# Performance work log

Hardware: AMD Instinct MI355X
Metric: run time of the kernel (lower is better)

## Reference

```python
import jax, jax.numpy as jnp
import numpy as np

NUM_EXPERTS = 8
AUX_LOSS_COEF = 0.01


def setup_inputs() -> dict:
    key = jax.random.key(0)
    ks = jax.random.split(key, 5)
    B, S, D, E, H = 4, 2048, 1024, NUM_EXPERTS, 4096
    scale = 0.02  # typical init scale so gelu/softmax stay in sane ranges
    return {
        "hidden_states": jax.random.normal(ks[0], (B, S, D), dtype=jnp.float32),
        "router_w": jax.random.normal(ks[1], (D, E), dtype=jnp.float32) * scale,
        "router_b": jnp.zeros((E,), dtype=jnp.float32),
        "w1": jax.random.normal(ks[2], (E, D, H), dtype=jnp.float32) * scale,
        "b1": jnp.zeros((E, H), dtype=jnp.float32),
        "w2": jax.random.normal(ks[3], (E, H, D), dtype=jnp.float32) * scale,
        "b2": jnp.zeros((E, D), dtype=jnp.float32),
    }


def reference(hidden_states, router_w, router_b, w1, b1, w2, b2):
    B, S, D = hidden_states.shape
    E = w1.shape[0]
    x = hidden_states.reshape(-1, D)  # [T, D] flattened tokens

    # Switch router: top-1 expert, combine weight = softmax prob of chosen expert
    logits = x @ router_w + router_b                      # [T, E]
    probs = jax.nn.softmax(logits, axis=-1)               # [T, E]
    sel = jnp.argmax(logits, axis=-1)                     # [T] int
    gate = jnp.take_along_axis(probs, sel[:, None], axis=1)[:, 0]  # [T]

    # Expert FFNs: per-expert Linear -> gelu -> Linear, masked top-1 combine.
    # Loop is over the small fixed expert count (structurally distinct weights).
    out = jnp.zeros_like(x)
    for e in range(E):
        h = jax.nn.gelu(x @ w1[e] + b1[e])                # [T, H]
        ye = h @ w2[e] + b2[e]                            # [T, D]
        mask = (sel == e).astype(x.dtype)
        out = out + (mask * gate)[:, None] * ye

    # Switch load-balancing auxiliary loss
    mean_probs = probs.mean(axis=0)                       # [E]
    assignments = jnp.mean(jax.nn.one_hot(sel, E, dtype=x.dtype), axis=0)  # [E]
    aux_loss = jnp.sum(mean_probs * assignments) * E
    total_loss = AUX_LOSS_COEF * aux_loss

    return out.reshape(B, S, D), total_loss
```

## Files before the change

kernel.cpp:

```cpp
#include <hip/hip_runtime.h>
#include <cstdint>

typedef __bf16 bf16_t;
typedef __attribute__((ext_vector_type(8))) __bf16 bf16x8;
typedef __attribute__((ext_vector_type(4))) float f32x4;
typedef unsigned short ushort_t;

#define TOKENS 8192
#define DIM 1024
#define HID 4096
#define NEXP 8


__device__ __forceinline__ void gl_lds16(const void* g, void* l) {
  __builtin_amdgcn_global_load_lds(
      (__attribute__((address_space(1))) void*)(void*)g,
      (__attribute__((address_space(3))) void*)l, 16, 0, 0);
}

__device__ __forceinline__ float gelu_fast(float x) {
  float x2 = x * x;
  float z2 = x * (1.59576912f + 0.07135482f * x2);
  float e = __expf(-z2);
  return x * __builtin_amdgcn_rcpf(1.f + e);
}

template <int N>
__device__ __forceinline__ void pwait() {
  __builtin_amdgcn_sched_barrier(0);
  if constexpr (N == 4) asm volatile("s_waitcnt vmcnt(4)" ::: "memory");
  else asm volatile("s_waitcnt vmcnt(0)" ::: "memory");
  __builtin_amdgcn_sched_barrier(0);
  __builtin_amdgcn_s_barrier();
  __builtin_amdgcn_sched_barrier(0);
}

__device__ __forceinline__ int xcd_chunk(int f, int nwg) {
  int q = nwg >> 3, r = nwg & 7;
  int xcd = f & 7, pos = f >> 3;
  return (xcd < r) ? (xcd * (q + 1) + pos) : (r * (q + 1) + (xcd - r) * q + pos);
}

__global__ void router_kernel(const float* __restrict__ x, const float* __restrict__ rw,
                              const float* __restrict__ rbias, bf16_t* __restrict__ xb,
                              int* __restrict__ sel, float* __restrict__ gate,
                              float* __restrict__ pprob, int* __restrict__ pcnt) {
  __shared__ float sprob[NEXP];
  __shared__ int scnt[NEXP];
  int t = threadIdx.x, lane = t & 63, wave = t >> 6;
  if (t < NEXP) { sprob[t] = 0.f; scnt[t] = 0; }
  __syncthreads();
  int tok = blockIdx.x * 4 + wave;
  const float* xp = x + (size_t)tok * DIM + lane * 16;
  float acc[NEXP];
#pragma unroll
  for (int e = 0; e < NEXP; ++e) acc[e] = 0.f;
  ushort_t xv[16];
#pragma unroll
  for (int j = 0; j < 16; j += 4) {
    float4 v = *(const float4*)(xp + j);
    const float* wr = rw + (size_t)(lane * 16 + j) * NEXP;
    float c[4] = {v.x, v.y, v.z, v.w};
#pragma unroll
    for (int d = 0; d < 4; ++d) {
      xv[j + d] = __builtin_bit_cast(ushort_t, (bf16_t)c[d]);
#pragma unroll
      for (int e = 0; e < NEXP; ++e) acc[e] += c[d] * wr[d * NEXP + e];
    }
  }
  {
    uint4* xop = (uint4*)(xb + (size_t)tok * DIM + lane * 16);
    xop[0] = ((uint4*)xv)[0];
    xop[1] = ((uint4*)xv)[1];
  }
#pragma unroll
  for (int s = 1; s < 64; s <<= 1)
#pragma unroll
    for (int e = 0; e < NEXP; ++e) acc[e] += __shfl_xor(acc[e], s);
  if (lane == 0) {
    float lg[NEXP];
#pragma unroll
    for (int e = 0; e < NEXP; ++e) lg[e] = acc[e] + rbias[e];
    float mx = lg[0]; int am = 0;
#pragma unroll
    for (int e = 1; e < NEXP; ++e) if (lg[e] > mx) { mx = lg[e]; am = e; }
    float p[NEXP]; float se = 0.f;
#pragma unroll
    for (int e = 0; e < NEXP; ++e) { p[e] = __expf(lg[e] - mx); se += p[e]; }
    float inv = 1.f / se;
#pragma unroll
    for (int e = 0; e < NEXP; ++e) { p[e] *= inv; atomicAdd(&sprob[e], p[e]); }
    sel[tok] = am;
    gate[tok] = p[am];
    atomicAdd(&scnt[am], 1);
  }
  __syncthreads();
  if (t < NEXP) {
    pprob[blockIdx.x * NEXP + t] = sprob[t];
    pcnt[blockIdx.x * NEXP + t] = scnt[t];
  }
}

__global__ void tcvt2_kernel(const float* __restrict__ w1, const float* __restrict__ w2,
                             bf16_t* __restrict__ w1t, bf16_t* __restrict__ w2t) {
  __shared__ float tile[64][65];
  int y = blockIdx.y;
  int which = y >> 3, e = y & 7;
  int R = which ? HID : DIM;
  int C = which ? DIM : HID;
  const float* src = (which ? w2 : w1) + (size_t)e * R * C;
  bf16_t* dst = (which ? w2t : w1t) + (size_t)e * R * C;
  int cbt = C >> 6;
  int rt = blockIdx.x / cbt, ct = blockIdx.x % cbt;
  int rb = rt * 64, cb = ct * 64;
  int t = threadIdx.x;
  int r = t >> 2, cq = (t & 3) * 16;
  const float* sp = src + (size_t)(rb + r) * C + cb + cq;
#pragma unroll
  for (int j = 0; j < 16; j += 4) {
    float4 v = *(const float4*)(sp + j);
    tile[r][cq + j + 0] = v.x; tile[r][cq + j + 1] = v.y;
    tile[r][cq + j + 2] = v.z; tile[r][cq + j + 3] = v.w;
  }
  __syncthreads();
  int oc = t >> 2, orr = (t & 3) * 16;
  ushort_t tmp[16];
#pragma unroll
  for (int j = 0; j < 16; ++j) {
    bf16_t b = (bf16_t)tile[orr + j][oc];
    tmp[j] = __builtin_bit_cast(ushort_t, b);
  }
  uint4* dp = (uint4*)(dst + (size_t)(cb + oc) * R + rb + orr);
  dp[0] = ((uint4*)tmp)[0];
  dp[1] = ((uint4*)tmp)[1];
}

__global__ void reduce_kernel(const float* __restrict__ pprob, const int* __restrict__ pcnt,
                              int nb, int* __restrict__ meta, float* __restrict__ loss_out) {
  __shared__ float fred[256];
  __shared__ int ired[256];
  int t = threadIdx.x;
  int e = t & 7, i0 = t >> 3;
  float fs = 0.f; int is = 0;
  for (int i = i0; i < nb; i += 32) { fs += pprob[i * 8 + e]; is += pcnt[i * 8 + e]; }
  fred[t] = fs; ired[t] = is;
  __syncthreads();
  if (t < NEXP) {
    float tp = 0.f; int tc = 0;
    for (int j = 0; j < 32; ++j) { tp += fred[j * 8 + t]; tc += ired[j * 8 + t]; }
    meta[t] = tc;
    fred[t] = tp;
    meta[16 + t] = 0;
  }
  __syncthreads();
  if (t == 0) {
    int off = 0; float loss = 0.f; int s2 = 0;
    for (int q = 0; q < NEXP; ++q) {
      int c = meta[q];
      meta[8 + q] = off;
      int nt2 = (c + 127) >> 7;
      for (int m = 0; m < nt2; ++m) meta[96 + s2++] = (q << 16) | m;
      off += c;
      loss += (fred[q] / (float)TOKENS) * ((float)c / (float)TOKENS);
    }
    meta[25] = s2;
    *loss_out = loss * (float)NEXP * 0.01f;
  }
}

__global__ void scatter_kernel(const int* __restrict__ sel, int* __restrict__ meta,
                               int* __restrict__ idxl) {
  int tok = blockIdx.x * 256 + threadIdx.x;
  int lane = threadIdx.x & 63;
  int e = sel[tok];
  const int* offsets = meta + 8;
  int* cursors = meta + 16;
#pragma unroll
  for (int ex = 0; ex < NEXP; ++ex) {
    unsigned long long mask = __ballot(e == ex);
    if (e == ex) {
      int leader = __ffsll(mask) - 1;
      int total = __popcll(mask);
      int rank = __popcll(mask & ((1ull << lane) - 1ull));
      int base = 0;
      if (lane == leader) base = atomicAdd(&cursors[ex], total);
      base = __shfl(base, leader);
      idxl[offsets[ex] + base + rank] = tok;
    }
  }
}

#define STG(Q, KT) do {                                                      \
    int _kb = (KT) * 32;                                                     \
    gl_lds16(apA0 + _kb, L + (Q) * 8192 + wave * 512);                       \
    gl_lds16(apA1 + _kb, L + (Q) * 8192 + 2048 + wave * 512);                 \
    gl_lds16(bpB0 + _kb, L + (Q) * 8192 + 4096 + wave * 512);                 \
    gl_lds16(bpB1 + _kb, L + (Q) * 8192 + 6144 + wave * 512);                 \
  } while (0)

#define CMP(Q) do {                                                          \
    const bf16_t* Ab = L + (Q) * 8192;                                       \
    const bf16_t* Bb = Ab + 4096;                                            \
    bf16x8 af[4], bv[4];                                                     \
    _Pragma("unroll")                                                        \
    for (int m = 0; m < 4; ++m)                                              \
      af[m] = *(const bf16x8*)&Ab[(wrow * 64 + m * 16 + l15) * 32 + ks];     \
    _Pragma("unroll")                                                        \
    for (int n = 0; n < 4; ++n)                                              \
      bv[n] = *(const bf16x8*)&Bb[(wcol * 64 + n * 16 + l15) * 32 + ks];     \
    __builtin_amdgcn_s_setprio(1);                                           \
    _Pragma("unroll")                                                        \
    for (int m = 0; m < 4; ++m)                                              \
      _Pragma("unroll")                                                      \
      for (int n = 0; n < 4; ++n)                                            \
        acc[m][n] = __builtin_amdgcn_mfma_f32_16x16x32_bf16(af[m], bv[n], acc[m][n], 0, 0, 0); \
    __builtin_amdgcn_s_setprio(0);                                           \
  } while (0)

__global__ __launch_bounds__(256, 3) void gemm1_kernel(
    const bf16_t* __restrict__ xb, const bf16_t* __restrict__ w1t,
    const float* __restrict__ b1, const int* __restrict__ idxl,
    const int* __restrict__ meta, bf16_t* __restrict__ h) {
  int S = gridDim.x;
  int f = blockIdx.y * S + blockIdx.x;
  int lf = xcd_chunk(f, S * gridDim.y);
  int slot = lf % S, nt = lf / S;
  if (slot >= meta[25]) return;
  int tm = meta[96 + slot];
  int e = tm >> 16, mt = tm & 0xffff;
  int cnt = meta[e];
  int off = meta[8 + e];
  int mBase = mt * 128;
  int nBase = nt * 128;
  __shared__ bf16_t L[24576];
  int t = threadIdx.x, lane = t & 63, wave = t >> 6;
  int l15 = lane & 15, g = lane >> 4;
  int wrow = wave >> 1, wcol = wave & 1;
  int ks = (g ^ (l15 & 3)) * 8;
  f32x4 acc[4][4];
#pragma unroll
  for (int m = 0; m < 4; ++m)
#pragma unroll
    for (int n = 0; n < 4; ++n) acc[m][n] = (f32x4){0.f, 0.f, 0.f, 0.f};

  int srow = t >> 2;
  int koff = ((t & 3) ^ (srow & 3)) * 8;
  int c1 = cnt - 1;
  int sA0 = mBase + srow; sA0 = sA0 < c1 ? sA0 : c1;
  int sA1 = mBase + 64 + srow; sA1 = sA1 < c1 ? sA1 : c1;
  const bf16_t* apA0 = xb + (size_t)idxl[off + sA0] * DIM + koff;
  const bf16_t* apA1 = xb + (size_t)idxl[off + sA1] * DIM + koff;
  const bf16_t* wb = w1t + (size_t)e * HID * DIM;
  const bf16_t* bpB0 = wb + (size_t)(nBase + srow) * DIM + koff;
  const bf16_t* bpB1 = wb + (size_t)(nBase + 64 + srow) * DIM + koff;

  STG(0, 0);
  STG(1, 1);
  pwait<4>();
#pragma unroll 1
  for (int kt = 0; kt < 30; kt += 3) {
    STG(2, kt + 2); CMP(0); pwait<4>();
    STG(0, kt + 3); CMP(1); pwait<4>();
    STG(1, kt + 4); CMP(2); pwait<4>();
  }
  CMP(0);
  pwait<0>();
  CMP(1);

  float bias[4];
#pragma unroll
  for (int n = 0; n < 4; ++n) bias[n] = b1[e * HID + nBase + wcol * 64 + n * 16 + l15];
#pragma unroll
  for (int m = 0; m < 4; ++m) {
    int rb0 = mBase + wrow * 64 + m * 16 + g * 4;
#pragma unroll
    for (int j = 0; j < 4; ++j) {
      int r = rb0 + j;
      if (r < cnt) {
        bf16_t* hp = h + (size_t)(off + r) * HID + nBase + wcol * 64 + l15;
#pragma unroll
        for (int n = 0; n < 4; ++n)
          hp[n * 16] = (bf16_t)gelu_fast(acc[m][n][j] + bias[n]);
      }
    }
  }
}

__global__ __launch_bounds__(256, 3) void gemm2_kernel(
    const bf16_t* __restrict__ h, const bf16_t* __restrict__ w2t,
    const float* __restrict__ b2, const int* __restrict__ idxl,
    const float* __restrict__ gate, const int* __restrict__ meta,
    float* __restrict__ out) {
  int S = gridDim.x;
  int f = blockIdx.y * S + blockIdx.x;
  int lf = xcd_chunk(f, S * gridDim.y);
  int slot = lf % S, nt = lf / S;
  if (slot >= meta[25]) return;
  int tm = meta[96 + slot];
  int e = tm >> 16, mt = tm & 0xffff;
  int cnt = meta[e];
  int off = meta[8 + e];
  int mBase = mt * 128;
  int nBase = nt * 128;
  __shared__ bf16_t L[24576];
  int t = threadIdx.x, lane = t & 63, wave = t >> 6;
  int l15 = lane & 15, g = lane >> 4;
  int wrow = wave >> 1, wcol = wave & 1;
  int ks = (g ^ (l15 & 3)) * 8;
  f32x4 acc[4][4];
#pragma unroll
  for (int m = 0; m < 4; ++m)
#pragma unroll
    for (int n = 0; n < 4; ++n) acc[m][n] = (f32x4){0.f, 0.f, 0.f, 0.f};

  int srow = t >> 2;
  int koff = ((t & 3) ^ (srow & 3)) * 8;
  int c1 = cnt - 1;
  int sA0 = mBase + srow; sA0 = sA0 < c1 ? sA0 : c1;
  int sA1 = mBase + 64 + srow; sA1 = sA1 < c1 ? sA1 : c1;
  const bf16_t* apA0 = h + (size_t)(off + sA0) * HID + koff;
  const bf16_t* apA1 = h + (size_t)(off + sA1) * HID + koff;
  const bf16_t* wb = w2t + (size_t)e * DIM * HID;
  const bf16_t* bpB0 = wb + (size_t)(nBase + srow) * HID + koff;
  const bf16_t* bpB1 = wb + (size_t)(nBase + 64 + srow) * HID + koff;

  STG(0, 0);
  STG(1, 1);
  pwait<4>();
#pragma unroll 1
  for (int kt = 0; kt < 126; kt += 3) {
    STG(2, kt + 2); CMP(0); pwait<4>();
    STG(0, kt + 3); CMP(1); pwait<4>();
    STG(1, kt + 4); CMP(2); pwait<4>();
  }
  CMP(0);
  pwait<0>();
  CMP(1);

  float bias[4];
#pragma unroll
  for (int n = 0; n < 4; ++n) bias[n] = b2[e * DIM + nBase + wcol * 64 + n * 16 + l15];
#pragma unroll
  for (int m = 0; m < 4; ++m) {
    int rb0 = mBase + wrow * 64 + m * 16 + g * 4;
#pragma unroll
    for (int j = 0; j < 4; ++j) {
      int r = rb0 + j;
      if (r < cnt) {
        int tok = idxl[off + r];
        float gg = gate[tok];
        float* op = out + (size_t)tok * DIM + nBase + wcol * 64 + l15;
#pragma unroll
        for (int n = 0; n < 4; ++n)
          op[n * 16] = gg * (acc[m][n][j] + bias[n]);
      }
    }
  }
}

extern "C" void kernel_launch(void* const* d_in, const int* in_sizes, int n_in,
                              void* d_out, int out_size, void* d_ws, size_t ws_size,
                              hipStream_t stream) {
  const float* hs = (const float*)d_in[0];
  const float* rw = (const float*)d_in[1];
  const float* rb = (const float*)d_in[2];
  const float* w1 = (const float*)d_in[3];
  const float* b1 = (const float*)d_in[4];
  const float* w2 = (const float*)d_in[5];
  const float* b2 = (const float*)d_in[6];
  float* out = (float*)d_out;
  char* ws = (char*)d_ws;

  bf16_t* xb   = (bf16_t*)(ws + 0);
  bf16_t* w1t  = (bf16_t*)(ws + 16777216);
  bf16_t* w2t  = (bf16_t*)(ws + 83886080);
  bf16_t* hbuf = (bf16_t*)(ws + 150994944);
  int*   sel   = (int*)  (ws + 220200960);
  float* gate  = (float*)(ws + 220233728);
  int*   idxl  = (int*)  (ws + 220266496);
  float* pprob = (float*)(ws + 220299264);
  int*   pcnt  = (int*)  (ws + 220364800);
  int*   meta  = (int*)  (ws + 220430336);

  router_kernel<<<2048, 256, 0, stream>>>(hs, rw, rb, xb, sel, gate, pprob, pcnt);
  tcvt2_kernel<<<dim3(1024, 16), 256, 0, stream>>>(w1, w2, w1t, w2t);
  reduce_kernel<<<1, 256, 0, stream>>>(pprob, pcnt, 2048, meta, out + (out_size - 1));
  scatter_kernel<<<32, 256, 0, stream>>>(sel, meta, idxl);
  gemm1_kernel<<<dim3(72, 32), 256, 0, stream>>>(xb, w1t, b1, idxl, meta, hbuf);
  gemm2_kernel<<<dim3(72, 8), 256, 0, stream>>>(hbuf, w2t, b2, idxl, gate, meta, out);
}
```

Measured before the change: 401.8 us.

## Fuse router and weight conversion kernels; enlarge gemm1 M-tile to 256 with 512 threads

The router and weight transpose/convert kernels are merged into one prep launch, with block ranges selecting the role. gemm1 now uses 256-row M tiles with 8 waves per block, so each block loads a single 128-row weight tile per stage and reuses it across more tokens. reduce_kernel builds a separate 256-row tile schedule for gemm1. This cuts weight traffic per token and one launch, at the cost of more LDS, padding waste on partial expert tiles and fewer blocks for gemm1.

```diff
diff --git a/kernel.cpp b/kernel.cpp
--- a/kernel.cpp
+++ b/kernel.cpp
@@ -29,6 +29,7 @@
 __device__ __forceinline__ void pwait() {
   __builtin_amdgcn_sched_barrier(0);
   if constexpr (N == 4) asm volatile("s_waitcnt vmcnt(4)" ::: "memory");
+  else if constexpr (N == 3) asm volatile("s_waitcnt vmcnt(3)" ::: "memory");
   else asm volatile("s_waitcnt vmcnt(0)" ::: "memory");
   __builtin_amdgcn_sched_barrier(0);
   __builtin_amdgcn_s_barrier();
@@ -41,98 +42,101 @@
   return (xcd < r) ? (xcd * (q + 1) + pos) : (r * (q + 1) + (xcd - r) * q + pos);
 }
 
-__global__ void router_kernel(const float* __restrict__ x, const float* __restrict__ rw,
-                              const float* __restrict__ rbias, bf16_t* __restrict__ xb,
-                              int* __restrict__ sel, float* __restrict__ gate,
-                              float* __restrict__ pprob, int* __restrict__ pcnt) {
-  __shared__ float sprob[NEXP];
-  __shared__ int scnt[NEXP];
-  int t = threadIdx.x, lane = t & 63, wave = t >> 6;
-  if (t < NEXP) { sprob[t] = 0.f; scnt[t] = 0; }
-  __syncthreads();
-  int tok = blockIdx.x * 4 + wave;
-  const float* xp = x + (size_t)tok * DIM + lane * 16;
-  float acc[NEXP];
-#pragma unroll
-  for (int e = 0; e < NEXP; ++e) acc[e] = 0.f;
-  ushort_t xv[16];
-#pragma unroll
-  for (int j = 0; j < 16; j += 4) {
-    float4 v = *(const float4*)(xp + j);
-    const float* wr = rw + (size_t)(lane * 16 + j) * NEXP;
-    float c[4] = {v.x, v.y, v.z, v.w};
-#pragma unroll
-    for (int d = 0; d < 4; ++d) {
-      xv[j + d] = __builtin_bit_cast(ushort_t, (bf16_t)c[d]);
-#pragma unroll
-      for (int e = 0; e < NEXP; ++e) acc[e] += c[d] * wr[d * NEXP + e];
-    }
-  }
-  {
-    uint4* xop = (uint4*)(xb + (size_t)tok * DIM + lane * 16);
-    xop[0] = ((uint4*)xv)[0];
-    xop[1] = ((uint4*)xv)[1];
-  }
-#pragma unroll
-  for (int s = 1; s < 64; s <<= 1)
-#pragma unroll
-    for (int e = 0; e < NEXP; ++e) acc[e] += __shfl_xor(acc[e], s);
-  if (lane == 0) {
-    float lg[NEXP];
-#pragma unroll
-    for (int e = 0; e < NEXP; ++e) lg[e] = acc[e] + rbias[e];
-    float mx = lg[0]; int am = 0;
-#pragma unroll
-    for (int e = 1; e < NEXP; ++e) if (lg[e] > mx) { mx = lg[e]; am = e; }
-    float p[NEXP]; float se = 0.f;
-#pragma unroll
-    for (int e = 0; e < NEXP; ++e) { p[e] = __expf(lg[e] - mx); se += p[e]; }
-    float inv = 1.f / se;
-#pragma unroll
-    for (int e = 0; e < NEXP; ++e) { p[e] *= inv; atomicAdd(&sprob[e], p[e]); }
-    sel[tok] = am;
-    gate[tok] = p[am];
-    atomicAdd(&scnt[am], 1);
-  }
-  __syncthreads();
-  if (t < NEXP) {
-    pprob[blockIdx.x * NEXP + t] = sprob[t];
-    pcnt[blockIdx.x * NEXP + t] = scnt[t];
-  }
-}
-
-__global__ void tcvt2_kernel(const float* __restrict__ w1, const float* __restrict__ w2,
-                             bf16_t* __restrict__ w1t, bf16_t* __restrict__ w2t) {
-  __shared__ float tile[64][65];
-  int y = blockIdx.y;
-  int which = y >> 3, e = y & 7;
-  int R = which ? HID : DIM;
-  int C = which ? DIM : HID;
-  const float* src = (which ? w2 : w1) + (size_t)e * R * C;
-  bf16_t* dst = (which ? w2t : w1t) + (size_t)e * R * C;
-  int cbt = C >> 6;
-  int rt = blockIdx.x / cbt, ct = blockIdx.x % cbt;
-  int rb = rt * 64, cb = ct * 64;
+__global__ void prep_kernel(const float* __restrict__ w1, const float* __restrict__ w2,
+                            bf16_t* __restrict__ w1t, bf16_t* __restrict__ w2t,
+                            const float* __restrict__ x, const float* __restrict__ rw,
+                            const float* __restrict__ rbias, bf16_t* __restrict__ xb,
+                            int* __restrict__ sel, float* __restrict__ gate,
+                            float* __restrict__ pprob, int* __restrict__ pcnt) {
+  int bid = blockIdx.x;
   int t = threadIdx.x;
-  int r = t >> 2, cq = (t & 3) * 16;
-  const float* sp = src + (size_t)(rb + r) * C + cb + cq;
-#pragma unroll
-  for (int j = 0; j < 16; j += 4) {
-    float4 v = *(const float4*)(sp + j);
-    tile[r][cq + j + 0] = v.x; tile[r][cq + j + 1] = v.y;
-    tile[r][cq + j + 2] = v.z; tile[r][cq + j + 3] = v.w;
-  }
-  __syncthreads();
-  int oc = t >> 2, orr = (t & 3) * 16;
-  ushort_t tmp[16];
-#pragma unroll
-  for (int j = 0; j < 16; ++j) {
-    bf16_t b = (bf16_t)tile[orr + j][oc];
-    tmp[j] = __builtin_bit_cast(ushort_t, b);
-  }
-  uint4* dp = (uint4*)(dst + (size_t)(cb + oc) * R + rb + orr);
-  dp[0] = ((uint4*)tmp)[0];
-  dp[1] = ((uint4*)tmp)[1];
+  if (bid < 16384) {
+    __shared__ float tile[64][65];
+    int y = bid >> 10, xb_ = bid & 1023;
+    int which = y >> 3, e = y & 7;
+    int R = which ? HID : DIM;
+    int C = which ? DIM : HID;
+    const float* src = (which ? w2 : w1) + (size_t)e * R * C;
+    bf16_t* dst = (which ? w2t : w1t) + (size_t)e * R * C;
+    int cbt = C >> 6;
+    int rt = xb_ / cbt, ct = xb_ % cbt;
+    int rb = rt * 64, cb = ct * 64;
+    int r = t >> 2, cq = (t & 3) * 16;
+    const float* sp = src + (size_t)(rb + r) * C + cb + cq;
+#pragma unroll
+    for (int j = 0; j < 16; j += 4) {
+      float4 v = *(const float4*)(sp + j);
+      tile[r][cq + j + 0] = v.x; tile[r][cq + j + 1] = v.y;
+      tile[r][cq + j + 2] = v.z; tile[r][cq + j + 3] = v.w;
+    }
+    __syncthreads();
+    int oc = t >> 2, orr = (t & 3) * 16;
+    ushort_t tmp[16];
+#pragma unroll
+    for (int j = 0; j < 16; ++j) {
+      bf16_t b = (bf16_t)tile[orr + j][oc];
+      tmp[j] = __builtin_bit_cast(ushort_t, b);
+    }
+    uint4* dp = (uint4*)(dst + (size_t)(cb + oc) * R + rb + orr);
+    dp[0] = ((uint4*)tmp)[0];
+    dp[1] = ((uint4*)tmp)[1];
+  } else {
+    __shared__ float sprob[NEXP];
+    __shared__ int scnt[NEXP];
+    int rblk = bid - 16384;
+    int lane = t & 63, wave = t >> 6;
+    if (t < NEXP) { sprob[t] = 0.f; scnt[t] = 0; }
+    __syncthreads();
+    int tok = rblk * 4 + wave;
+    const float* xp = x + (size_t)tok * DIM + lane * 16;
+    float acc[NEXP];
+#pragma unroll
+    for (int e = 0; e < NEXP; ++e) acc[e] = 0.f;
+    ushort_t xv[16];
+#pragma unroll
+    for (int j = 0; j < 16; j += 4) {
+      float4 v = *(const float4*)(xp + j);
+      const float* wr = rw + (size_t)(lane * 16 + j) * NEXP;
+      float c[4] = {v.x, v.y, v.z, v.w};
+#pragma unroll
+      for (int d = 0; d < 4; ++d) {
+        xv[j + d] = __builtin_bit_cast(ushort_t, (bf16_t)c[d]);
+#pragma unroll
+        for (int e = 0; e < NEXP; ++e) acc[e] += c[d] * wr[d * NEXP + e];
+      }
+    }
+    {
+      uint4* xop = (uint4*)(xb + (size_t)tok * DIM + lane * 16);
+      xop[0] = ((uint4*)xv)[0];
+      xop[1] = ((uint4*)xv)[1];
+    }
+#pragma unroll
+    for (int s = 1; s < 64; s <<= 1)
+#pragma unroll
+      for (int e = 0; e < NEXP; ++e) acc[e] += __shfl_xor(acc[e], s);
+    if (lane == 0) {
+      float lg[NEXP];
+#pragma unroll
+      for (int e = 0; e < NEXP; ++e) lg[e] = acc[e] + rbias[e];
+      float mx = lg[0]; int am = 0;
+#pragma unroll
+      for (int e = 1; e < NEXP; ++e) if (lg[e] > mx) { mx = lg[e]; am = e; }
+      float p[NEXP]; float se = 0.f;
+#pragma unroll
+      for (int e = 0; e < NEXP; ++e) { p[e] = __expf(lg[e] - mx); se += p[e]; }
+      float inv = 1.f / se;
+#pragma unroll
+      for (int e = 0; e < NEXP; ++e) { p[e] *= inv; atomicAdd(&sprob[e], p[e]); }
+      sel[tok] = am;
+      gate[tok] = p[am];
+      atomicAdd(&scnt[am], 1);
+    }
+    __syncthreads();
+    if (t < NEXP) {
+      pprob[rblk * NEXP + t] = sprob[t];
+      pcnt[rblk * NEXP + t] = scnt[t];
+    }
+  }
 }
 
 __global__ void reduce_kernel(const float* __restrict__ pprob, const int* __restrict__ pcnt,
@@ -154,15 +158,18 @@
   }
   __syncthreads();
   if (t == 0) {
-    int off = 0; float loss = 0.f; int s2 = 0;
+    int off = 0; float loss = 0.f; int s1 = 0, s2 = 0;
     for (int q = 0; q < NEXP; ++q) {
       int c = meta[q];
       meta[8 + q] = off;
+      int nt1 = (c + 255) >> 8;
+      for (int m = 0; m < nt1; ++m) meta[32 + s1++] = (q << 16) | m;
       int nt2 = (c + 127) >> 7;
       for (int m = 0; m < nt2; ++m) meta[96 + s2++] = (q << 16) | m;
       off += c;
       loss += (fred[q] / (float)TOKENS) * ((float)c / (float)TOKENS);
     }
+    meta[24] = s1;
     meta[25] = s2;
     *loss_out = loss * (float)NEXP * 0.01f;
   }
@@ -190,17 +197,16 @@
   }
 }
 
-#define STG(Q, KT) do {                                                      \
+#define STG1(Q, KT) do {                                                     \
     int _kb = (KT) * 32;                                                     \
-    gl_lds16(apA0 + _kb, L + (Q) * 8192 + wave * 512);                       \
-    gl_lds16(apA1 + _kb, L + (Q) * 8192 + 2048 + wave * 512);                 \
-    gl_lds16(bpB0 + _kb, L + (Q) * 8192 + 4096 + wave * 512);                 \
-    gl_lds16(bpB1 + _kb, L + (Q) * 8192 + 6144 + wave * 512);                 \
+    gl_lds16(apA0 + _kb, L + (Q) * 12288 + wave * 512);                      \
+    gl_lds16(apA1 + _kb, L + (Q) * 12288 + 4096 + wave * 512);               \
+    gl_lds16(bpB0 + _kb, L + (Q) * 12288 + 8192 + wave * 512);               \
   } while (0)
 
-#define CMP(Q) do {                                                          \
-    const bf16_t* Ab = L + (Q) * 8192;                                       \
-    const bf16_t* Bb = Ab + 4096;                                            \
+#define CMP1(Q) do {                                                         \
+    const bf16_t* Ab = L + (Q) * 12288;                                      \
+    const bf16_t* Bb = Ab + 8192;                                            \
     bf16x8 af[4], bv[4];                                                     \
     _Pragma("unroll")                                                        \
     for (int m = 0; m < 4; ++m)                                              \
@@ -217,7 +223,7 @@
     __builtin_amdgcn_s_setprio(0);                                           \
   } while (0)
 
-__global__ __launch_bounds__(256, 3) void gemm1_kernel(
+__global__ __launch_bounds__(512, 4) void gemm1_kernel(
     const bf16_t* __restrict__ xb, const bf16_t* __restrict__ w1t,
     const float* __restrict__ b1, const int* __restrict__ idxl,
     const int* __restrict__ meta, bf16_t* __restrict__ h) {
@@ -225,14 +231,14 @@
   int f = blockIdx.y * S + blockIdx.x;
   int lf = xcd_chunk(f, S * gridDim.y);
   int slot = lf % S, nt = lf / S;
-  if (slot >= meta[25]) return;
-  int tm = meta[96 + slot];
+  if (slot >= meta[24]) return;
+  int tm = meta[32 + slot];
   int e = tm >> 16, mt = tm & 0xffff;
   int cnt = meta[e];
   int off = meta[8 + e];
-  int mBase = mt * 128;
+  int mBase = mt * 256;
   int nBase = nt * 128;
-  __shared__ bf16_t L[24576];
+  __shared__ bf16_t L[36864];
   int t = threadIdx.x, lane = t & 63, wave = t >> 6;
   int l15 = lane & 15, g = lane >> 4;
   int wrow = wave >> 1, wcol = wave & 1;
@@ -247,25 +253,24 @@
   int koff = ((t & 3) ^ (srow & 3)) * 8;
   int c1 = cnt - 1;
   int sA0 = mBase + srow; sA0 = sA0 < c1 ? sA0 : c1;
-  int sA1 = mBase + 64 + srow; sA1 = sA1 < c1 ? sA1 : c1;
+  int sA1 = mBase + 128 + srow; sA1 = sA1 < c1 ? sA1 : c1;
   const bf16_t* apA0 = xb + (size_t)idxl[off + sA0] * DIM + koff;
   const bf16_t* apA1 = xb + (size_t)idxl[off + sA1] * DIM + koff;
   const bf16_t* wb = w1t + (size_t)e * HID * DIM;
   const bf16_t* bpB0 = wb + (size_t)(nBase + srow) * DIM + koff;
-  const bf16_t* bpB1 = wb + (size_t)(nBase + 64 + srow) * DIM + koff;
-
-  STG(0, 0);
-  STG(1, 1);
-  pwait<4>();
+
+  STG1(0, 0);
+  STG1(1, 1);
+  pwait<3>();
 #pragma unroll 1
   for (int kt = 0; kt < 30; kt += 3) {
-    STG(2, kt + 2); CMP(0); pwait<4>();
-    STG(0, kt + 3); CMP(1); pwait<4>();
-    STG(1, kt + 4); CMP(2); pwait<4>();
-  }
-  CMP(0);
+    STG1(2, kt + 2); CMP1(0); pwait<3>();
+    STG1(0, kt + 3); CMP1(1); pwait<3>();
+    STG1(1, kt + 4); CMP1(2); pwait<3>();
+  }
+  CMP1(0);
   pwait<0>();
-  CMP(1);
+  CMP1(1);
 
   float bias[4];
 #pragma unroll
@@ -285,6 +290,33 @@
     }
   }
 }
+
+#define STG2(Q, KT) do {                                                     \
+    int _kb = (KT) * 32;                                                     \
+    gl_lds16(apA0 + _kb, L + (Q) * 8192 + wave * 512);                       \
+    gl_lds16(apA1 + _kb, L + (Q) * 8192 + 2048 + wave * 512);                \
+    gl_lds16(bpB0 + _kb, L + (Q) * 8192 + 4096 + wave * 512);                \
+    gl_lds16(bpB1 + _kb, L + (Q) * 8192 + 6144 + wave * 512);                \
+  } while (0)
+
+#define CMP2(Q) do {                                                         \
+    const bf16_t* Ab = L + (Q) * 8192;                                       \
+    const bf16_t* Bb = Ab + 4096;                                            \
+    bf16x8 af[4], bv[4];                                                     \
+    _Pragma("unroll")                                                        \
+    for (int m = 0; m < 4; ++m)                                              \
+      af[m] = *(const bf16x8*)&Ab[(wrow * 64 + m * 16 + l15) * 32 + ks];     \
+    _Pragma("unroll")                                                        \
+    for (int n = 0; n < 4; ++n)                                              \
+      bv[n] = *(const bf16x8*)&Bb[(wcol * 64 + n * 16 + l15) * 32 + ks];     \
+    __builtin_amdgcn_s_setprio(1);                                           \
+    _Pragma("unroll")                                                        \
+    for (int m = 0; m < 4; ++m)                                              \
+      _Pragma("unroll")                                                      \
+      for (int n = 0; n < 4; ++n)                                            \
+        acc[m][n] = __builtin_amdgcn_mfma_f32_16x16x32_bf16(af[m], bv[n], acc[m][n], 0, 0, 0); \
+    __builtin_amdgcn_s_setprio(0);                                           \
+  } while (0)
 
 __global__ __launch_bounds__(256, 3) void gemm2_kernel(
     const bf16_t* __restrict__ h, const bf16_t* __restrict__ w2t,
@@ -324,18 +356,18 @@
   const bf16_t* bpB0 = wb + (size_t)(nBase + srow) * HID + koff;
   const bf16_t* bpB1 = wb + (size_t)(nBase + 64 + srow) * HID + koff;
 
-  STG(0, 0);
-  STG(1, 1);
+  STG2(0, 0);
+  STG2(1, 1);
   pwait<4>();
 #pragma unroll 1
   for (int kt = 0; kt < 126; kt += 3) {
-    STG(2, kt + 2); CMP(0); pwait<4>();
-    STG(0, kt + 3); CMP(1); pwait<4>();
-    STG(1, kt + 4); CMP(2); pwait<4>();
-  }
-  CMP(0);
+    STG2(2, kt + 2); CMP2(0); pwait<4>();
+    STG2(0, kt + 3); CMP2(1); pwait<4>();
+    STG2(1, kt + 4); CMP2(2); pwait<4>();
+  }
+  CMP2(0);
   pwait<0>();
-  CMP(1);
+  CMP2(1);
 
   float bias[4];
 #pragma unroll
@@ -382,10 +414,10 @@
   int*   pcnt  = (int*)  (ws + 220364800);
   int*   meta  = (int*)  (ws + 220430336);
 
-  router_kernel<<<2048, 256, 0, stream>>>(hs, rw, rb, xb, sel, gate, pprob, pcnt);
-  tcvt2_kernel<<<dim3(1024, 16), 256, 0, stream>>>(w1, w2, w1t, w2t);
+  prep_kernel<<<18432, 256, 0, stream>>>(w1, w2, w1t, w2t, hs, rw, rb, xb,
+                                         sel, gate, pprob, pcnt);
   reduce_kernel<<<1, 256, 0, stream>>>(pprob, pcnt, 2048, meta, out + (out_size - 1));
   scatter_kernel<<<32, 256, 0, stream>>>(sel, meta, idxl);
-  gemm1_kernel<<<dim3(72, 32), 256, 0, stream>>>(xb, w1t, b1, idxl, meta, hbuf);
+  gemm1_kernel<<<dim3(40, 32), 512, 0, stream>>>(xb, w1t, b1, idxl, meta, hbuf);
   gemm2_kernel<<<dim3(72, 8), 256, 0, stream>>>(hbuf, w2t, b2, idxl, gate, meta, out);
 }
```

After: 389.9 us. -2.9%, faster.
